# Kernel tuning notes

Hardware: AMD Instinct MI355X
Metric: run time of the kernel (lower is better)

## Reference

```python
import jax, jax.numpy as jnp
import numpy as np

Z_DIM = 2  # state dimension is hard-coded (fc1: Linear(2, H), fc3: Linear(H, 2))


def _mlp(z, W1, b1, W2, b2, W3, b3):
    # torch.nn.Linear: y = x @ W.T + b
    h = jax.nn.elu(z @ W1.T + b1)
    h = jax.nn.elu(h @ W2.T + b2)
    return h @ W3.T + b3


def setup_inputs() -> dict:
    key = jax.random.key(0)
    ks = jax.random.split(key, 8)
    B, H = 1_000_000, 64
    s_in = 1.0 / np.sqrt(Z_DIM)
    s_h = 1.0 / np.sqrt(H)
    u = lambda k, shp, s: jax.random.uniform(k, shp, jnp.float32, -s, s)
    return {
        "t": jax.random.normal(ks[0], (1,), jnp.float32),
        "z_and_logp": jax.random.normal(ks[1], (B, Z_DIM + 1), jnp.float32),
        "W1": u(ks[2], (H, Z_DIM), s_in),
        "b1": u(ks[3], (H,), s_in),
        "W2": u(ks[4], (H, H), s_h),
        "b2": u(ks[5], (H,), s_h),
        "W3": u(ks[6], (Z_DIM, H), s_h),
        "b3": u(ks[7], (Z_DIM,), s_h),
    }


def reference(t, z_and_logp, W1, b1, W2, b2, W3, b3):
    # t is an unused time argument (ODE solver interface).
    z = z_and_logp[:, :Z_DIM]  # [B, 2]; logp column is not used in forward
    f = lambda x: _mlp(x, W1, b1, W2, b2, W3, b3)

    # Exact Jacobian trace via forward-mode JVPs with unit tangents (Z_DIM=2,
    # so this small fixed loop mirrors the per-dim autograd loop in torch).
    dz_dt = None
    trace = jnp.zeros(z.shape[0], dtype=z.dtype)
    for i in range(Z_DIM):
        e = jnp.zeros_like(z).at[:, i].set(1.0)
        out, jz = jax.jvp(f, (z,), (e,))
        if dz_dt is None:
            dz_dt = out
        trace = trace + jz[:, i]

    dlogp_dt = -trace[:, None]  # [B, 1]
    return jnp.concatenate([dz_dt, dlogp_dt], axis=1)  # [B, 3]
```

## Files before the change

kernel.cpp:

```cpp
#include <hip/hip_runtime.h>
#include <hip/hip_bf16.h>


typedef short bf16x8 __attribute__((ext_vector_type(8)));
typedef float f32x4  __attribute__((ext_vector_type(4)));

static __device__ __forceinline__ short f2bf(float x) {
    __hip_bfloat16 b = __float2bfloat16(x);
    return __builtin_bit_cast(short, b);
}

__global__ __launch_bounds__(256) __attribute__((amdgpu_waves_per_eu(2, 2)))
void odefunc_mfma(const float* __restrict__ zin,
                  const float* __restrict__ W1, const float* __restrict__ b1,
                  const float* __restrict__ W2, const float* __restrict__ b2,
                  const float* __restrict__ W3, const float* __restrict__ b3,
                  float* __restrict__ out, int B, int ntiles)
{
    const int lane = threadIdx.x & 63;
    const int quad = lane >> 4;
    const int col  = lane & 15;

    const int wid    = blockIdx.x * (blockDim.x >> 6) + (threadIdx.x >> 6);
    const int nwaves = gridDim.x * (blockDim.x >> 6);

    bf16x8 aW2[4][2];
#pragma unroll
    for (int mt = 0; mt < 4; ++mt)
#pragma unroll
        for (int jt = 0; jt < 2; ++jt) {
            const float* p = W2 + (mt * 16 + col) * 64 + jt * 32 + quad * 8;
#pragma unroll
            for (int jj = 0; jj < 8; ++jj) aW2[mt][jt][jj] = f2bf(p[jj]);
        }

    float w0v[2][8], w1v[2][8], b1v[2][8];
#pragma unroll
    for (int jt = 0; jt < 2; ++jt)
#pragma unroll
        for (int jj = 0; jj < 8; ++jj) {
            int j = jt * 32 + quad * 8 + jj;
            w0v[jt][jj] = W1[2 * j];
            w1v[jt][jj] = W1[2 * j + 1];
            b1v[jt][jj] = b1[j];
        }

    float b2v[4][4], w30v[4][4], w31v[4][4];
#pragma unroll
    for (int mt = 0; mt < 4; ++mt)
#pragma unroll
        for (int i = 0; i < 4; ++i) {
            int k = mt * 16 + quad * 4 + i;
            b2v[mt][i]  = b2[k];
            w30v[mt][i] = W3[k];
            w31v[mt][i] = W3[64 + k];
        }
    const float b30 = b3[0], b31 = b3[1];
    const f32x4 zero4 = {0.f, 0.f, 0.f, 0.f};

    for (int t = wid; t < ntiles; t += nwaves) {
        int row = t * 16 + col;
        int rl = row < B ? row : B - 1;
        float z0 = zin[3 * rl + 0];
        float z1 = zin[3 * rl + 1];

        bf16x8 Ah[2], Au[2], Av[2];
#pragma unroll
        for (int jt = 0; jt < 2; ++jt)
#pragma unroll
            for (int jj = 0; jj < 8; ++jj) {
                float w0 = w0v[jt][jj], w1 = w1v[jt][jj];
                float a  = fmaf(w0, z0, fmaf(w1, z1, b1v[jt][jj]));
                float ex = __expf(fminf(a, 0.f));
                float h  = fmaxf(a, 0.f) + (ex - 1.f);
                Ah[jt][jj] = f2bf(h);
                Au[jt][jj] = f2bf(ex * w0);
                Av[jt][jj] = f2bf(ex * w1);
            }

        f32x4 accH[4], accU[4], accV[4];
#pragma unroll
        for (int mt = 0; mt < 4; ++mt) {
            accH[mt] = __builtin_amdgcn_mfma_f32_16x16x32_bf16(aW2[mt][0], Ah[0], zero4, 0, 0, 0);
            accH[mt] = __builtin_amdgcn_mfma_f32_16x16x32_bf16(aW2[mt][1], Ah[1], accH[mt], 0, 0, 0);
            accU[mt] = __builtin_amdgcn_mfma_f32_16x16x32_bf16(aW2[mt][0], Au[0], zero4, 0, 0, 0);
            accU[mt] = __builtin_amdgcn_mfma_f32_16x16x32_bf16(aW2[mt][1], Au[1], accU[mt], 0, 0, 0);
            accV[mt] = __builtin_amdgcn_mfma_f32_16x16x32_bf16(aW2[mt][0], Av[0], zero4, 0, 0, 0);
            accV[mt] = __builtin_amdgcn_mfma_f32_16x16x32_bf16(aW2[mt][1], Av[1], accV[mt], 0, 0, 0);
        }

        float o0 = 0.f, o1 = 0.f, trc = 0.f;
#pragma unroll
        for (int mt = 0; mt < 4; ++mt)
#pragma unroll
            for (int i = 0; i < 4; ++i) {
                float a2  = accH[mt][i] + b2v[mt][i];
                float ex2 = __expf(fminf(a2, 0.f));
                float hh  = fmaxf(a2, 0.f) + (ex2 - 1.f);
                o0  = fmaf(w30v[mt][i], hh, o0);
                o1  = fmaf(w31v[mt][i], hh, o1);
                trc = fmaf(ex2, fmaf(w30v[mt][i], accU[mt][i],
                                     w31v[mt][i] * accV[mt][i]), trc);
            }

        o0  += __shfl_xor(o0, 16);  o0  += __shfl_xor(o0, 32);
        o1  += __shfl_xor(o1, 16);  o1  += __shfl_xor(o1, 32);
        trc += __shfl_xor(trc, 16); trc += __shfl_xor(trc, 32);

        if (lane < 16 && row < B) {
            out[3 * row + 0] = o0 + b30;
            out[3 * row + 1] = o1 + b31;
            out[3 * row + 2] = -trc;
        }
    }
}

extern "C" void kernel_launch(void* const* d_in, const int* in_sizes, int n_in,
                              void* d_out, int out_size, void* d_ws, size_t ws_size,
                              hipStream_t stream) {
    const float* zin = (const float*)d_in[1];
    const float* W1  = (const float*)d_in[2];
    const float* b1  = (const float*)d_in[3];
    const float* W2  = (const float*)d_in[4];
    const float* b2  = (const float*)d_in[5];
    const float* W3  = (const float*)d_in[6];
    const float* b3  = (const float*)d_in[7];
    float* out = (float*)d_out;

    int B = in_sizes[1] / 3;
    int ntiles = (B + 15) / 16;
    int grid = 1024;
    odefunc_mfma<<<grid, 256, 0, stream>>>(zin, W1, b1, W2, b2, W3, b3,
                                           out, B, ntiles);
}
```

Measured before the change: 137.9 us.

## Move small weights to LDS, prefetch next tile, raise occupancy

Per-lane register copies of W1, b1, b2 and W3 are replaced by one shared-memory table that is read as vector loads inside the loop, which frees registers so occupancy can rise from 2 to 3 waves per EU, with the grid enlarged to match. The input for each tile is now read as one coalesced 48-float load per wave and spread with shuffles, and the next tile's load is issued one iteration ahead. In exchange the loop gains LDS reads and shuffles, and an empty asm barrier keeps the compiler from hoisting the LDS reads back into registers.

```diff
diff --git a/kernel.cpp b/kernel.cpp
--- a/kernel.cpp
+++ b/kernel.cpp
@@ -10,16 +10,29 @@
     return __builtin_bit_cast(short, b);
 }
 
-__global__ __launch_bounds__(256) __attribute__((amdgpu_waves_per_eu(2, 2)))
+__global__ __launch_bounds__(256) __attribute__((amdgpu_waves_per_eu(3, 3)))
 void odefunc_mfma(const float* __restrict__ zin,
                   const float* __restrict__ W1, const float* __restrict__ b1,
                   const float* __restrict__ W2, const float* __restrict__ b2,
                   const float* __restrict__ W3, const float* __restrict__ b3,
                   float* __restrict__ out, int B, int ntiles)
 {
+    __shared__ f32x4 sC[96];
+
     const int lane = threadIdx.x & 63;
     const int quad = lane >> 4;
     const int col  = lane & 15;
+
+    if (threadIdx.x < 64) {
+        int i = threadIdx.x;
+        float* s = (float*)sC;
+        s[i]       = W1[2*i];
+        s[64 + i]  = W1[2*i + 1];
+        s[128 + i] = b1[i];
+        s[192 + i] = b2[i];
+        s[256 + i] = W3[i];
+        s[320 + i] = W3[64 + i];
+    }
 
     const int wid    = blockIdx.x * (blockDim.x >> 6) + (threadIdx.x >> 6);
     const int nwaves = gridDim.x * (blockDim.x >> 6);
@@ -34,49 +47,47 @@
             for (int jj = 0; jj < 8; ++jj) aW2[mt][jt][jj] = f2bf(p[jj]);
         }
 
-    float w0v[2][8], w1v[2][8], b1v[2][8];
-#pragma unroll
-    for (int jt = 0; jt < 2; ++jt)
-#pragma unroll
-        for (int jj = 0; jj < 8; ++jj) {
-            int j = jt * 32 + quad * 8 + jj;
-            w0v[jt][jj] = W1[2 * j];
-            w1v[jt][jj] = W1[2 * j + 1];
-            b1v[jt][jj] = b1[j];
-        }
-
-    float b2v[4][4], w30v[4][4], w31v[4][4];
-#pragma unroll
-    for (int mt = 0; mt < 4; ++mt)
-#pragma unroll
-        for (int i = 0; i < 4; ++i) {
-            int k = mt * 16 + quad * 4 + i;
-            b2v[mt][i]  = b2[k];
-            w30v[mt][i] = W3[k];
-            w31v[mt][i] = W3[64 + k];
-        }
     const float b30 = b3[0], b31 = b3[1];
     const f32x4 zero4 = {0.f, 0.f, 0.f, 0.f};
 
-    for (int t = wid; t < ntiles; t += nwaves) {
-        int row = t * 16 + col;
-        int rl = row < B ? row : B - 1;
-        float z0 = zin[3 * rl + 0];
-        float z1 = zin[3 * rl + 1];
+    __syncthreads();
+
+    const int lload = lane < 48 ? lane : 47;
+    int t = wid;
+    float zv = 0.f;
+    if (t < ntiles) zv = zin[t * 48 + lload];
+
+    int cofs = 0;
+    for (; t < ntiles; t += nwaves) {
+        asm volatile("" : "+v"(cofs));
+
+        int tn = t + nwaves;
+        int tc = tn < ntiles ? tn : t;
+        float zvn = zin[tc * 48 + lload];
+
+        float z0 = __shfl(zv, 3 * col);
+        float z1 = __shfl(zv, 3 * col + 1);
 
         bf16x8 Ah[2], Au[2], Av[2];
 #pragma unroll
-        for (int jt = 0; jt < 2; ++jt)
+        for (int jt = 0; jt < 2; ++jt) {
+            int j4 = cofs + jt * 8 + quad * 2;
+            f32x4 w0a = sC[j4],      w0b = sC[j4 + 1];
+            f32x4 w1a = sC[j4 + 16], w1b = sC[j4 + 17];
+            f32x4 bba = sC[j4 + 32], bbb = sC[j4 + 33];
 #pragma unroll
             for (int jj = 0; jj < 8; ++jj) {
-                float w0 = w0v[jt][jj], w1 = w1v[jt][jj];
-                float a  = fmaf(w0, z0, fmaf(w1, z1, b1v[jt][jj]));
+                float w0 = (jj < 4) ? w0a[jj & 3] : w0b[jj & 3];
+                float w1 = (jj < 4) ? w1a[jj & 3] : w1b[jj & 3];
+                float bb = (jj < 4) ? bba[jj & 3] : bbb[jj & 3];
+                float a  = fmaf(w0, z0, fmaf(w1, z1, bb));
                 float ex = __expf(fminf(a, 0.f));
                 float h  = fmaxf(a, 0.f) + (ex - 1.f);
                 Ah[jt][jj] = f2bf(h);
                 Au[jt][jj] = f2bf(ex * w0);
                 Av[jt][jj] = f2bf(ex * w1);
             }
+        }
 
         f32x4 accH[4], accU[4], accV[4];
 #pragma unroll
@@ -91,27 +102,34 @@
 
         float o0 = 0.f, o1 = 0.f, trc = 0.f;
 #pragma unroll
-        for (int mt = 0; mt < 4; ++mt)
+        for (int mt = 0; mt < 4; ++mt) {
+            int k4 = cofs + 48 + mt * 4 + quad;
+            f32x4 b2v = sC[k4];
+            f32x4 w30 = sC[k4 + 16];
+            f32x4 w31 = sC[k4 + 32];
 #pragma unroll
             for (int i = 0; i < 4; ++i) {
-                float a2  = accH[mt][i] + b2v[mt][i];
+                float a2  = accH[mt][i] + b2v[i];
                 float ex2 = __expf(fminf(a2, 0.f));
                 float hh  = fmaxf(a2, 0.f) + (ex2 - 1.f);
-                o0  = fmaf(w30v[mt][i], hh, o0);
-                o1  = fmaf(w31v[mt][i], hh, o1);
-                trc = fmaf(ex2, fmaf(w30v[mt][i], accU[mt][i],
-                                     w31v[mt][i] * accV[mt][i]), trc);
+                o0  = fmaf(w30[i], hh, o0);
+                o1  = fmaf(w31[i], hh, o1);
+                trc = fmaf(ex2, fmaf(w30[i], accU[mt][i], w31[i] * accV[mt][i]), trc);
             }
+        }
 
         o0  += __shfl_xor(o0, 16);  o0  += __shfl_xor(o0, 32);
         o1  += __shfl_xor(o1, 16);  o1  += __shfl_xor(o1, 32);
         trc += __shfl_xor(trc, 16); trc += __shfl_xor(trc, 32);
 
+        int row = t * 16 + col;
         if (lane < 16 && row < B) {
             out[3 * row + 0] = o0 + b30;
             out[3 * row + 1] = o1 + b31;
             out[3 * row + 2] = -trc;
         }
+
+        zv = zvn;
     }
 }
 
@@ -129,7 +147,7 @@
 
     int B = in_sizes[1] / 3;
     int ntiles = (B + 15) / 16;
-    int grid = 1024;
+    int grid = 1536;
     odefunc_mfma<<<grid, 256, 0, stream>>>(zin, W1, b1, W2, b2, W3, b3,
                                            out, B, ntiles);
 }
```

Result: no change. 137.6 us (-0.3%).
